# Performance work log

Measured on AMD Instinct MI355X. Metric: run time of the kernel, lower is better.

Reference implementation:

```python
import jax, jax.numpy as jnp
import numpy as np

DM = 512; NH = 8; EL = 3; FACTOR = 3; EPS = 1e-5

def layernorm(x, g, b):
    m = x.mean(-1, keepdims=True)
    v = x.var(-1, keepdims=True)
    return (x - m) / jnp.sqrt(v + EPS) * g + b

def pos_embed(L, d):
    pos = jnp.arange(L, dtype=jnp.float32)[:, None]
    div = jnp.exp(jnp.arange(0, d, 2, dtype=jnp.float32) * (-np.log(10000.0) / d))
    pe = jnp.zeros((L, d), jnp.float32)
    pe = pe.at[:, 0::2].set(jnp.sin(pos * div))
    pe = pe.at[:, 1::2].set(jnp.cos(pos * div))
    return pe

def circ_conv1d(x, w, b=None):
    # x: [B,L,Cin], w: [Cout,Cin,3]; torch Conv1d padding=1, padding_mode='circular'
    xp = jnp.concatenate([x[:, -1:], x, x[:, :1]], axis=1)
    y = jax.lax.conv_general_dilated(xp, w, (1,), 'VALID', dimension_numbers=('NWC', 'OIW', 'NWC'))
    return y if b is None else y + b

def prob_attention(q, k, v, rng):
    # q,k,v: [B,H,L,D] -- Informer ProbSparse attention (non-masked encoder case)
    B, H, L, D = q.shape
    LK = k.shape[2]
    U = min(int(FACTOR * np.ceil(np.log(LK))), LK)   # sampled keys per query
    u = min(int(FACTOR * np.ceil(np.log(L))), L)     # top queries kept
    idx = jax.random.randint(rng, (L, U), 0, LK)     # shared across B,H as in torch
    k_samp = k[:, :, idx]                            # [B,H,L,U,D]
    qk = jnp.einsum('bhld,bhlud->bhlu', q, k_samp)
    M = qk.max(-1) - qk.sum(-1) / LK                 # sparsity measure
    top = jax.lax.top_k(M, u)[1]                     # [B,H,u]
    q_red = jnp.take_along_axis(q, top[..., None], axis=2)
    scores = jnp.einsum('bhud,bhkd->bhuk', q_red, k) / jnp.sqrt(jnp.asarray(D, q.dtype))
    attn = jax.nn.softmax(scores, axis=-1)
    upd = jnp.einsum('bhuk,bhkd->bhud', attn, v)
    ctx = jnp.broadcast_to(v.mean(axis=2, keepdims=True), (B, H, L, D))
    bi = jnp.arange(B)[:, None, None]
    hi = jnp.arange(H)[None, :, None]
    return ctx.at[bi, hi, top].set(upd)

def encoder_layer(x, p, rng):
    Wq_, bq_, Wk_, bk_, Wv_, bv_, Wo_, bo_, w1, b1, w2, b2, g1, be1, g2, be2 = p
    B, L, _ = x.shape
    D = DM // NH
    q = (x @ Wq_.T + bq_).reshape(B, L, NH, D).transpose(0, 2, 1, 3)
    k = (x @ Wk_.T + bk_).reshape(B, L, NH, D).transpose(0, 2, 1, 3)
    v = (x @ Wv_.T + bv_).reshape(B, L, NH, D).transpose(0, 2, 1, 3)
    ctx = prob_attention(q, k, v, rng).transpose(0, 2, 1, 3).reshape(B, L, DM)
    x = x + (ctx @ Wo_.T + bo_)
    x = layernorm(x, g1, be1)
    y = jax.nn.gelu(x @ w1.T + b1, approximate=False)  # pointwise conv1 (k=1)
    y = y @ w2.T + b2                                   # pointwise conv2 (k=1)
    return layernorm(x + y, g2, be2)

def distil_layer(x, w, b, g, beta):
    y = circ_conv1d(x, w, b)                 # Conv1d k=3 circular
    mu = y.mean((0, 1))
    var = y.var((0, 1))                      # BatchNorm1d, training stats
    y = (y - mu) / jnp.sqrt(var + EPS) * g + beta
    y = jax.nn.elu(y)
    # MaxPool1d(kernel=3, stride=2, padding=1)
    return jax.lax.reduce_window(y, -jnp.inf, jax.lax.max, (1, 3, 1), (1, 2, 1), ((0, 0), (1, 1), (0, 0)))

def setup_inputs():
    key = jax.random.key(0)
    ks = jax.random.split(key, 12)
    B, S, CIN, COUT, DFF = 8, 2048, 7, 7, 2048
    r = lambda k, s: jax.random.normal(k, s, jnp.float32)
    return {
        'x_enc': r(ks[0], (B, S, CIN)),
        'tok_w': r(ks[1], (DM, CIN, 3)) * (2.0 / (CIN * 3)) ** 0.5,
        'Wq': r(ks[2], (EL, DM, DM)) * DM ** -0.5, 'bq': jnp.zeros((EL, DM)),
        'Wk': r(ks[3], (EL, DM, DM)) * DM ** -0.5, 'bk': jnp.zeros((EL, DM)),
        'Wv': r(ks[4], (EL, DM, DM)) * DM ** -0.5, 'bv': jnp.zeros((EL, DM)),
        'Wo': r(ks[5], (EL, DM, DM)) * DM ** -0.5, 'bo': jnp.zeros((EL, DM)),
        'conv1_w': r(ks[6], (EL, DFF, DM)) * DM ** -0.5, 'conv1_b': jnp.zeros((EL, DFF)),
        'conv2_w': r(ks[7], (EL, DM, DFF)) * DFF ** -0.5, 'conv2_b': jnp.zeros((EL, DM)),
        'ln1_g': jnp.ones((EL, DM)), 'ln1_b': jnp.zeros((EL, DM)),
        'ln2_g': jnp.ones((EL, DM)), 'ln2_b': jnp.zeros((EL, DM)),
        'dconv_w': r(ks[8], (EL - 1, DM, DM, 3)) * (DM * 3) ** -0.5, 'dconv_b': jnp.zeros((EL - 1, DM)),
        'bn_g': jnp.ones((EL - 1, DM)), 'bn_b': jnp.zeros((EL - 1, DM)),
        'lnf_g': jnp.ones((DM,)), 'lnf_b': jnp.zeros((DM,)),
        'end_w': r(ks[9], (COUT, DM)) * DM ** -0.5, 'end_b': jnp.zeros((COUT,)),
    }

def reference(x_enc, tok_w, Wq, bq, Wk, bk, Wv, bv, Wo, bo, conv1_w, conv1_b, conv2_w, conv2_b, ln1_g, ln1_b, ln2_g, ln2_b, dconv_w, dconv_b, bn_g, bn_b, lnf_g, lnf_b, end_w, end_b):
    x = circ_conv1d(x_enc, tok_w) + pos_embed(x_enc.shape[1], DM)  # DataEmbedding
    base = jax.random.key(42)
    for l in range(EL):
        p = (Wq[l], bq[l], Wk[l], bk[l], Wv[l], bv[l], Wo[l], bo[l],
             conv1_w[l], conv1_b[l], conv2_w[l], conv2_b[l],
             ln1_g[l], ln1_b[l], ln2_g[l], ln2_b[l])
        x = encoder_layer(x, p, jax.random.fold_in(base, l))
        if l < EL - 1:
            x = distil_layer(x, dconv_w[l], dconv_b[l], bn_g[l], bn_b[l])
    x = layernorm(x, lnf_g, lnf_b)
    return x @ end_w.T + end_b  # end_conv2 (Conv1d k=1)
```

## Files before the change

kernel.cpp:

```cpp
#include <hip/hip_runtime.h>
#include <cstdint>
#include <cstddef>

#define DMODEL 512
#define NHEAD 8
#define HD 64

typedef float f32x4 __attribute__((ext_vector_type(4)));
typedef _Float16 f16x8 __attribute__((ext_vector_type(8)));
typedef _Float16 f16x4 __attribute__((ext_vector_type(4)));

__device__ __forceinline__ uint32_t rotl32(uint32_t x, int r) {
  return (x << r) | (x >> (32 - r));
}

__device__ __forceinline__ void tf_block(uint32_t k0, uint32_t k1,
                                         uint32_t& x0, uint32_t& x1) {
  uint32_t ks0 = k0, ks1 = k1, ks2 = k0 ^ k1 ^ 0x1BD11BDAu;
  x0 += ks0; x1 += ks1;
  x0 += x1; x1 = rotl32(x1, 13); x1 ^= x0;
  x0 += x1; x1 = rotl32(x1, 15); x1 ^= x0;
  x0 += x1; x1 = rotl32(x1, 26); x1 ^= x0;
  x0 += x1; x1 = rotl32(x1, 6);  x1 ^= x0;
  x0 += ks1; x1 += ks2 + 1u;
  x0 += x1; x1 = rotl32(x1, 17); x1 ^= x0;
  x0 += x1; x1 = rotl32(x1, 29); x1 ^= x0;
  x0 += x1; x1 = rotl32(x1, 16); x1 ^= x0;
  x0 += x1; x1 = rotl32(x1, 24); x1 ^= x0;
  x0 += ks2; x1 += ks0 + 2u;
  x0 += x1; x1 = rotl32(x1, 13); x1 ^= x0;
  x0 += x1; x1 = rotl32(x1, 15); x1 ^= x0;
  x0 += x1; x1 = rotl32(x1, 26); x1 ^= x0;
  x0 += x1; x1 = rotl32(x1, 6);  x1 ^= x0;
  x0 += ks0; x1 += ks1 + 3u;
  x0 += x1; x1 = rotl32(x1, 17); x1 ^= x0;
  x0 += x1; x1 = rotl32(x1, 29); x1 ^= x0;
  x0 += x1; x1 = rotl32(x1, 16); x1 ^= x0;
  x0 += x1; x1 = rotl32(x1, 24); x1 ^= x0;
  x0 += ks1; x1 += ks2 + 4u;
  x0 += x1; x1 = rotl32(x1, 13); x1 ^= x0;
  x0 += x1; x1 = rotl32(x1, 15); x1 ^= x0;
  x0 += x1; x1 = rotl32(x1, 26); x1 ^= x0;
  x0 += x1; x1 = rotl32(x1, 6);  x1 ^= x0;
  x0 += ks2; x1 += ks0 + 5u;
}

__global__ void idx_kernel(int* __restrict__ idxb, int n, int layer, int mask) {
  int e = blockIdx.x * 256 + threadIdx.x;
  if (e >= n) return;
  uint32_t f0 = 0u, f1 = (uint32_t)layer;
  tf_block(0u, 42u, f0, f1);
  uint32_t s0 = 0u, s1 = 1u;
  tf_block(f0, f1, s0, s1);
  uint32_t x0 = 0u, x1 = (uint32_t)e;
  tf_block(s0, s1, x0, x1);
  uint32_t bits = x0 ^ x1;
  idxb[e] = (int)(bits & (uint32_t)mask);
}

__device__ __forceinline__ float gelu_f(float v) {
  return 0.5f * v * (1.0f + erff(v * 0.7071067811865476f));
}

template <int ACT, int HASR, int CONV, int PART>
__global__ __launch_bounds__(256, 2) void gemm128(
    const float* __restrict__ A, const void* __restrict__ Wsp,
    const float* __restrict__ bias, const float* Rres, float* C,
    int N, int K, int Lmask, int ntx, int nty, int kloop, int ks) {
  __shared__ __align__(16) _Float16 sm[4][128][32];
  const _Float16* Wh = (const _Float16*)Wsp;
  const _Float16* Wl = Wh + (size_t)N * K;
  const int tid = threadIdx.x;
  int blk = blockIdx.x;
  const int tiles = ntx * nty;
  int kb = 0;
  if (PART) { kb = blk / tiles; blk -= kb * tiles; }
  const int koff = kb * kloop;
  const int xcd = blk & 7;
  const int j = blk >> 3;
  const int jr = j / ntx;
  const int row_t = xcd * (nty >> 3) + jr;
  const int col_t = j - jr * ntx;
  const int row0 = row_t * 128, col0 = col_t * 128;

  const int r4 = tid >> 2;
  const int ss = tid & 3;

  const float* Ap0 = A + (size_t)(row0 + r4) * K + koff + ss * 8;
  const float* Ap1 = A + (size_t)(row0 + 64 + r4) * K + koff + ss * 8;
  const _Float16* Wh0 = Wh + (size_t)(col0 + r4) * K + koff + ss * 8;
  const _Float16* Wh1 = Wh + (size_t)(col0 + 64 + r4) * K + koff + ss * 8;
  const _Float16* Wl0 = Wl + (size_t)(col0 + r4) * K + koff + ss * 8;
  const _Float16* Wl1 = Wl + (size_t)(col0 + 64 + r4) * K + koff + ss * 8;
  int tcv0 = 0, bb0 = 0, tcv1 = 0, bb1 = 0;
  if (CONV) {
    int a0 = row0 + r4, a1 = row0 + 64 + r4;
    tcv0 = a0 & Lmask; bb0 = a0 & ~Lmask;
    tcv1 = a1 & Lmask; bb1 = a1 & ~Lmask;
  }

  const int lane = tid & 63;
  const int wv = tid >> 6;
  const int wr = (wv >> 1) << 6;
  const int wc = (wv & 1) << 6;
  const int fr = lane & 15;
  const int fs = lane >> 4;

  f32x4 acc[4][4];
  {
    f32x4 z = {0.f, 0.f, 0.f, 0.f};
#pragma unroll
    for (int r = 0; r < 4; ++r)
#pragma unroll
      for (int c = 0; c < 4; ++c) acc[r][c] = z;
  }

  f32x4 ra[4], rwh[2], rwl[2];

  auto gload = [&](int k0) {
    const float *a0p, *a1p;
    if (CONV) {
      int kabs = koff + k0 + ss * 8;
      int w = kabs >> 9, cq = kabs & 511;
      a0p = A + (size_t)(bb0 | ((tcv0 - 1 + w) & Lmask)) * 512 + cq;
      a1p = A + (size_t)(bb1 | ((tcv1 - 1 + w) & Lmask)) * 512 + cq;
    } else {
      a0p = Ap0 + k0;
      a1p = Ap1 + k0;
    }
    ra[0] = *(const f32x4*)(a0p);
    ra[1] = *(const f32x4*)(a0p + 4);
    ra[2] = *(const f32x4*)(a1p);
    ra[3] = *(const f32x4*)(a1p + 4);
    rwh[0] = *(const f32x4*)(Wh0 + k0);
    rwh[1] = *(const f32x4*)(Wh1 + k0);
    rwl[0] = *(const f32x4*)(Wl0 + k0);
    rwl[1] = *(const f32x4*)(Wl1 + k0);
  };

  const int T = kloop >> 5;
  gload(0);

  for (int it = 0; it < T; ++it) {
#pragma unroll
    for (int p = 0; p < 2; ++p) {
      const int row = (p << 6) + r4;
      const int sl = (ss ^ ((row >> 1) & 3)) << 3;
      float tmp[8];
      *(f32x4*)(tmp) = ra[2 * p];
      *(f32x4*)(tmp + 4) = ra[2 * p + 1];
      _Float16 hv[8], lv[8];
#pragma unroll
      for (int q = 0; q < 8; ++q) {
        _Float16 h = (_Float16)tmp[q];
        hv[q] = h;
        lv[q] = (_Float16)(tmp[q] - (float)h);
      }
      *(f16x8*)&sm[0][row][sl] = *(f16x8*)hv;
      *(f16x8*)&sm[1][row][sl] = *(f16x8*)lv;
      *(f32x4*)&sm[2][row][sl] = rwh[p];
      *(f32x4*)&sm[3][row][sl] = rwl[p];
    }
    __syncthreads();
    if (it + 1 < T) gload((it + 1) << 5);
    f16x8 wfh[4], wfl[4], afh[4], afl[4];
#pragma unroll
    for (int c = 0; c < 4; ++c) {
      const int row = wc + (c << 4) + fr;
      const int sl = (fs ^ ((row >> 1) & 3)) << 3;
      wfh[c] = *(const f16x8*)&sm[2][row][sl];
      wfl[c] = *(const f16x8*)&sm[3][row][sl];
    }
#pragma unroll
    for (int r = 0; r < 4; ++r) {
      const int row = wr + (r << 4) + fr;
      const int sl = (fs ^ ((row >> 1) & 3)) << 3;
      afh[r] = *(const f16x8*)&sm[0][row][sl];
      afl[r] = *(const f16x8*)&sm[1][row][sl];
    }
#pragma unroll
    for (int r = 0; r < 4; ++r)
#pragma unroll
      for (int c = 0; c < 4; ++c) {
        acc[r][c] = __builtin_amdgcn_mfma_f32_16x16x32_f16(afh[r], wfh[c],
                                                           acc[r][c], 0, 0, 0);
        acc[r][c] = __builtin_amdgcn_mfma_f32_16x16x32_f16(afh[r], wfl[c],
                                                           acc[r][c], 0, 0, 0);
        acc[r][c] = __builtin_amdgcn_mfma_f32_16x16x32_f16(afl[r], wfh[c],
                                                           acc[r][c], 0, 0, 0);
      }
    __syncthreads();
  }

  const int crow = fs << 2;
  if (PART) {
    float* Cp = C + (size_t)kb * ((size_t)(nty << 7)) * N;
#pragma unroll
    for (int r = 0; r < 4; ++r) {
      const int m0 = row0 + wr + (r << 4) + crow;
#pragma unroll
      for (int c = 0; c < 4; ++c) {
        const int n0 = col0 + wc + (c << 4) + fr;
#pragma unroll
        for (int q = 0; q < 4; ++q)
          Cp[(size_t)(m0 + q) * N + n0] = acc[r][c][q];
      }
    }
  } else {
#pragma unroll
    for (int r = 0; r < 4; ++r) {
      const int m0 = row0 + wr + (r << 4) + crow;
#pragma unroll
      for (int c = 0; c < 4; ++c) {
        const int n0 = col0 + wc + (c << 4) + fr;
        const float bcol = bias[n0];
#pragma unroll
        for (int q = 0; q < 4; ++q) {
          float v = acc[r][c][q] + bcol;
          if (HASR) v += Rres[(size_t)(m0 + q) * N + n0];
          if (ACT == 1) v = gelu_f(v);
          C[(size_t)(m0 + q) * N + n0] = v;
        }
      }
    }
  }
}

template <int HASR>
__global__ __launch_bounds__(256) void combine_kernel(
    const float* __restrict__ part, const float* __restrict__ bias,
    const float* Rres, float* __restrict__ Cout, size_t MN, int ks) {
  size_t gid = (size_t)blockIdx.x * 256 + threadIdx.x;
  int c = (int)(gid & 511);
  float v = 0.f;
  for (int kb = 0; kb < ks; kb++) v += part[kb * MN + gid];
  v += bias[c];
  if (HASR) v += Rres[gid];
  Cout[gid] = v;
}

__global__ __launch_bounds__(256) void splitw_kernel(const float* __restrict__ w,
                                                     _Float16* __restrict__ o,
                                                     int n) {
  int g = (blockIdx.x * 256 + threadIdx.x) << 2;
  if (g >= n) return;
  f32x4 f = *(const f32x4*)(w + g);
  f16x4 hv, lv;
#pragma unroll
  for (int q = 0; q < 4; ++q) {
    _Float16 h = (_Float16)f[q];
    hv[q] = h;
    lv[q] = (_Float16)(f[q] - (float)h);
  }
  *(f16x4*)(o + g) = hv;
  *(f16x4*)(o + n + g) = lv;
}

__global__ void tokpe_kernel(const float* __restrict__ xe,
                             const float* __restrict__ w,
                             float* __restrict__ out, int S) {
  int gid = blockIdx.x * 256 + threadIdx.x;
  int o = gid & 511;
  int bt = gid >> 9;
  int t = bt % S, b = bt / S;
  float acc = 0.f;
#pragma unroll
  for (int ww = 0; ww < 3; ww++) {
    int tt = t - 1 + ww;
    tt = (tt < 0) ? tt + S : (tt >= S ? tt - S : tt);
    const float* xr = xe + ((size_t)(b * S + tt)) * 7;
#pragma unroll
    for (int i = 0; i < 7; i++) acc += xr[i] * w[o * 21 + i * 3 + ww];
  }
  int i2 = o >> 1;
  float dv = expf((float)(2 * i2) * (-9.210340371976184f / 512.0f));
  float ang = (float)t * dv;
  acc += (o & 1) ? cosf(ang) : sinf(ang);
  out[gid] = acc;
}

__global__ void packw_kernel(const float* __restrict__ dw,
                             _Float16* __restrict__ wp) {
  int gid = blockIdx.x * 256 + threadIdx.x;
  int o = gid / 1536;
  int kk = gid - o * 1536;
  int ww = kk / 512;
  int c = kk - ww * 512;
  float v = dw[((size_t)o * 512 + c) * 3 + ww];
  _Float16 h = (_Float16)v;
  wp[gid] = h;
  wp[786432 + gid] = (_Float16)(v - (float)h);
}

__global__ __launch_bounds__(256, 8) void mscore_kernel(
    const float* __restrict__ Q, const float* __restrict__ Kb,
    const int* __restrict__ idxb, float* __restrict__ Mout, int L, int U) {
  int i = blockIdx.x;
  int b = i & 7;
  int j = i >> 3;
  int tid = threadIdx.x;
  int qd = tid >> 2;
  int q = tid & 3;
  int h = qd & 7;
  int t = j * 8 + (qd >> 3);
  const float* qp = Q + ((size_t)(b * L + t)) * DMODEL + h * HD + q * 4;
  float4 qv0 = *(const float4*)(qp);
  float4 qv1 = *(const float4*)(qp + 16);
  float4 qv2 = *(const float4*)(qp + 32);
  float4 qv3 = *(const float4*)(qp + 48);
  const float* Kh = Kb + (size_t)b * L * DMODEL + h * HD + q * 4;
  const int* ip = idxb + t * U;
  float mx = -3.4e38f, sm = 0.f;
  int kr = ip[0];
  for (int jj = 0; jj < U; jj++) {
    const float* kp = Kh + (size_t)kr * DMODEL;
    float4 k0 = *(const float4*)(kp);
    float4 k1 = *(const float4*)(kp + 16);
    float4 k2 = *(const float4*)(kp + 32);
    float4 k3 = *(const float4*)(kp + 48);
    if (jj + 1 < U) kr = ip[jj + 1];
    float d = qv0.x * k0.x + qv0.y * k0.y + qv0.z * k0.z + qv0.w * k0.w +
              qv1.x * k1.x + qv1.y * k1.y + qv1.z * k1.z + qv1.w * k1.w +
              qv2.x * k2.x + qv2.y * k2.y + qv2.z * k2.z + qv2.w * k2.w +
              qv3.x * k3.x + qv3.y * k3.y + qv3.z * k3.z + qv3.w * k3.w;
    d += __shfl_xor(d, 1);
    d += __shfl_xor(d, 2);
    mx = fmaxf(mx, d);
    sm += d;
  }
  if (q == 0) Mout[(size_t)(b * 8 + h) * L + t] = mx - sm / (float)L;
}

__global__ __launch_bounds__(256) void topk_kernel(const float* __restrict__ Mv,
                                                   int* __restrict__ topb, int L,
                                                   int u) {
  __shared__ float wv_s[4];
  __shared__ int wi_s[4];
  __shared__ int best_s;
// ... 332 lines not shown
    if (t < 0 || t >= L) continue;
    float yv = (z[((size_t)(b * L + t)) * DMODEL + c] - m) * inv * gg + bb;
    yv = (yv > 0.f) ? yv : expm1f(yv);
    best = fmaxf(best, yv);
  }
  out[gid] = best;
}

__global__ __launch_bounds__(64) void end_kernel(const float* __restrict__ xn,
                                                 const float* __restrict__ ew,
                                                 const float* __restrict__ eb,
                                                 float* __restrict__ out) {
  __shared__ float xs[512];
  __shared__ float red[64];
  int row = blockIdx.x, tid = threadIdx.x;
#pragma unroll
  for (int i = 0; i < 8; i++) xs[tid + 64 * i] = xn[(size_t)row * DMODEL + tid + 64 * i];
  __syncthreads();
  for (int c = 0; c < 7; c++) {
    float p = 0.f;
    for (int d = tid; d < 512; d += 64) p += xs[d] * ew[c * DMODEL + d];
    red[tid] = p;
    __syncthreads();
    for (int s = 32; s > 0; s >>= 1) {
      if (tid < s) red[tid] += red[tid + s];
      __syncthreads();
    }
    if (tid == 0) out[row * 7 + c] = red[0] + eb[c];
    __syncthreads();
  }
}

extern "C" void kernel_launch(void* const* d_in, const int* in_sizes, int n_in,
                              void* d_out, int out_size, void* d_ws,
                              size_t ws_size, hipStream_t stream) {
  (void)in_sizes; (void)n_in; (void)out_size;
  const float* x_enc = (const float*)d_in[0];
  const float* tok_w = (const float*)d_in[1];
  const float* Wq = (const float*)d_in[2];
  const float* bq = (const float*)d_in[3];
  const float* Wk = (const float*)d_in[4];
  const float* bk = (const float*)d_in[5];
  const float* Wv = (const float*)d_in[6];
  const float* bv = (const float*)d_in[7];
  const float* Wo = (const float*)d_in[8];
  const float* bo = (const float*)d_in[9];
  const float* w1 = (const float*)d_in[10];
  const float* b1 = (const float*)d_in[11];
  const float* w2 = (const float*)d_in[12];
  const float* b2 = (const float*)d_in[13];
  const float* g1 = (const float*)d_in[14];
  const float* be1 = (const float*)d_in[15];
  const float* g2 = (const float*)d_in[16];
  const float* be2 = (const float*)d_in[17];
  const float* dw = (const float*)d_in[18];
  const float* db = (const float*)d_in[19];
  const float* bng = (const float*)d_in[20];
  const float* bnb = (const float*)d_in[21];
  const float* lnfg = (const float*)d_in[22];
  const float* lnfb = (const float*)d_in[23];
  const float* endw = (const float*)d_in[24];
  const float* endb = (const float*)d_in[25];
  float* out = (float*)d_out;
  char* ws = (char*)d_ws;

  const int NCHMAX = 32;

  size_t o = 0;
  float* buf0 = (float*)(ws + o); o += (size_t)16384 * 512 * 4;
  float* qbuf = (float*)(ws + o); o += (size_t)16384 * 512 * 4;
  float* kbuf = (float*)(ws + o); o += (size_t)16384 * 512 * 4;
  float* wpack = (float*)(ws + o); o += (size_t)512 * 1536 * 4;
  float* Mb    = (float*)(ws + o); o += (size_t)64 * 2048 * 4;
  int*   idxb  = (int*)(ws + o);   o += (size_t)2048 * 24 * 4;
  int*   topb  = (int*)(ws + o);   o += 8192;
  float* qsel  = (float*)(ws + o); o += (size_t)64 * 24 * 64 * 4;
  float* mvg   = (float*)(ws + o); o += (size_t)8 * 512 * 4;
  float* mvWog = (float*)(ws + o); o += (size_t)8 * 512 * 4;
  float* psumx = (float*)(ws + o); o += (size_t)64 * 512 * 4;
  float* psum  = (float*)(ws + o); o += (size_t)128 * 512 * 4;
  float* psq   = (float*)(ws + o); o += (size_t)128 * 512 * 4;
  float* muv   = (float*)(ws + o); o += 2048;
  float* varv  = (float*)(ws + o); o += 2048;
  float* pmb   = (float*)(ws + o); o += (size_t)64 * NCHMAX * 24 * 4;
  float* plb   = (float*)(ws + o); o += (size_t)64 * NCHMAX * 24 * 4;
  float* pOb   = (float*)(ws + o); o += (size_t)64 * NCHMAX * 24 * 64 * 4;
  _Float16* wqs = (_Float16*)(ws + o); o += (size_t)512 * 512 * 4;
  _Float16* w1s = (_Float16*)(ws + o); o += (size_t)2048 * 512 * 4;
  _Float16* w2s = (_Float16*)(ws + o); o += (size_t)512 * 2048 * 4;
  float* partb = (float*)(ws + o); o += (size_t)4 * 4096 * 2048;
  const bool uks = (ws_size >= o);

  const int B = 8;
  const int S = 2048;
  tokpe_kernel<<<B * S * DMODEL / 256, 256, 0, stream>>>(x_enc, tok_w, buf0, S);

  int L = S;
  const int Uarr[3] = {24, 21, 21};
  for (int l = 0; l < 3; l++) {
    int U = Uarr[l];
    int u = Uarr[l];
    int BL = B * L;
    int nty = BL / 128;
    size_t MN = (size_t)BL * 512;
    int gq = 4 * nty;
    int ksq = (gq >= 512 || !uks) ? 1 : (512 / gq);
    int nch = L >> 6;
    idx_kernel<<<(L * U + 255) / 256, 256, 0, stream>>>(idxb, L * U, l, L - 1);

    splitw_kernel<<<256, 256, 0, stream>>>(Wq + (size_t)l * 262144, wqs, 262144);
    if (ksq == 1) {
      gemm128<0, 0, 0, 0><<<gq, 256, 0, stream>>>(
          buf0, wqs, bq + l * 512, nullptr, qbuf, 512, 512, 0, 4, nty, 512, 1);
    } else {
      gemm128<0, 0, 0, 1><<<gq * ksq, 256, 0, stream>>>(
          buf0, wqs, nullptr, nullptr, partb, 512, 512, 0, 4, nty, 512 / ksq,
          ksq);
      combine_kernel<0><<<(unsigned)(MN / 256), 256, 0, stream>>>(
          partb, bq + l * 512, nullptr, qbuf, MN, ksq);
    }
    splitw_kernel<<<256, 256, 0, stream>>>(Wk + (size_t)l * 262144, wqs, 262144);
    if (ksq == 1) {
      gemm128<0, 0, 0, 0><<<gq, 256, 0, stream>>>(
          buf0, wqs, bk + l * 512, nullptr, kbuf, 512, 512, 0, 4, nty, 512, 1);
    } else {
      gemm128<0, 0, 0, 1><<<gq * ksq, 256, 0, stream>>>(
          buf0, wqs, nullptr, nullptr, partb, 512, 512, 0, 4, nty, 512 / ksq,
          ksq);
      combine_kernel<0><<<(unsigned)(MN / 256), 256, 0, stream>>>(
          partb, bk + l * 512, nullptr, kbuf, MN, ksq);
    }
    mscore_kernel<<<L, 256, 0, stream>>>(qbuf, kbuf, idxb, Mb, L, U);
    topk_kernel<<<64, 256, 0, stream>>>(Mb, topb, L, u);
    gatherq_kernel<<<64 * u, 64, 0, stream>>>(qbuf, topb, qsel, L, u);
    xmean_kernel<<<64, 256, 0, stream>>>(buf0, psumx, L);
    mvmake_kernel<<<8, 256, 0, stream>>>(psumx, Wv + (size_t)l * 262144,
                                         bv + l * 512, Wo + (size_t)l * 262144,
                                         bo + l * 512, mvg, mvWog, L);
    splitw_kernel<<<256, 256, 0, stream>>>(Wv + (size_t)l * 262144, wqs, 262144);
    if (ksq == 1) {
      gemm128<0, 0, 0, 0><<<gq, 256, 0, stream>>>(
          buf0, wqs, bv + l * 512, nullptr, qbuf, 512, 512, 0, 4, nty, 512, 1);
    } else {
      gemm128<0, 0, 0, 1><<<gq * ksq, 256, 0, stream>>>(
          buf0, wqs, nullptr, nullptr, partb, 512, 512, 0, 4, nty, 512 / ksq,
          ksq);
      combine_kernel<0><<<(unsigned)(MN / 256), 256, 0, stream>>>(
          partb, bv + l * 512, nullptr, qbuf, MN, ksq);
    }
    attnflash_kernel<<<64 * nch, 256, 0, stream>>>(qsel, kbuf, qbuf, pmb, plb,
                                                   pOb, L, u, nch);
    x1bcast_kernel<<<(unsigned)(MN / 256), 256, 0, stream>>>(buf0, mvWog, kbuf, L);
    deltaWo_kernel<<<64 * u, 256, 0, stream>>>(pmb, plb, pOb, mvg, topb,
                                               Wo + (size_t)l * 262144, kbuf, L,
                                               u, nch);
    ln_kernel<<<BL / 4, 256, 0, stream>>>(kbuf, g1 + l * 512, be1 + l * 512, qbuf);
    splitw_kernel<<<1024, 256, 0, stream>>>(w1 + (size_t)l * 1048576, w1s,
                                            1048576);
    splitw_kernel<<<1024, 256, 0, stream>>>(w2 + (size_t)l * 1048576, w2s,
                                            1048576);
    for (int r0 = 0; r0 < BL; r0 += 4096) {
      gemm128<1, 0, 0, 0><<<16 * 32, 256, 0, stream>>>(
          qbuf + (size_t)r0 * 512, w1s, b1 + l * 2048, nullptr, buf0, 2048, 512,
          0, 16, 32, 512, 1);
      if (uks) {
        gemm128<0, 0, 0, 1><<<4 * 32 * 4, 256, 0, stream>>>(
            buf0, w2s, nullptr, nullptr, partb, 512, 2048, 0, 4, 32, 512, 4);
        combine_kernel<1><<<4096 * 512 / 256, 256, 0, stream>>>(
            partb, b2 + l * 512, qbuf + (size_t)r0 * 512,
            kbuf + (size_t)r0 * 512, (size_t)4096 * 512, 4);
      } else {
        gemm128<0, 1, 0, 0><<<4 * 32, 256, 0, stream>>>(
            buf0, w2s, b2 + l * 512, qbuf + (size_t)r0 * 512,
            kbuf + (size_t)r0 * 512, 512, 2048, 0, 4, 32, 2048, 1);
      }
    }
    ln_kernel<<<BL / 4, 256, 0, stream>>>(kbuf, g2 + l * 512, be2 + l * 512, buf0);

    if (l < 2) {
      packw_kernel<<<512 * 1536 / 256, 256, 0, stream>>>(
          dw + (size_t)l * 512 * 512 * 3, (_Float16*)wpack);
      int ksc = (gq >= 512 || !uks) ? 1 : 2;
      if (ksc == 1) {
        gemm128<0, 0, 1, 0><<<gq, 256, 0, stream>>>(
            buf0, wpack, db + l * 512, nullptr, kbuf, 512, 1536, L - 1, 4, nty,
            1536, 1);
      } else {
        gemm128<0, 0, 1, 1><<<gq * 2, 256, 0, stream>>>(
            buf0, wpack, nullptr, nullptr, partb, 512, 1536, L - 1, 4, nty, 768,
            2);
        combine_kernel<0><<<(unsigned)(MN / 256), 256, 0, stream>>>(
            partb, db + l * 512, nullptr, kbuf, MN, 2);
      }
      int nb = BL / 128;
      bnpart_kernel<<<nb, 256, 0, stream>>>(kbuf, psum, psq, 128);
      bnfin_kernel<<<2, 256, 0, stream>>>(psum, psq, muv, varv, nb, BL);
      bnpool_kernel<<<(BL / 2) * 512 / 256, 256, 0, stream>>>(
          kbuf, muv, varv, bng + l * 512, bnb + l * 512, buf0, L);
      L >>= 1;
    }
  }
  int BL = B * L;
  ln_kernel<<<BL / 4, 256, 0, stream>>>(buf0, lnfg, lnfb, qbuf);
  end_kernel<<<BL, 64, 0, stream>>>(qbuf, endw, endb, out);
}
```

Measured before the change: 1.970 ms.

## Double-buffer LDS tiles in gemm128 to overlap staging with MFMA

Splits the GEMM shared memory into two buffers so the next K-slice is converted and written to LDS while MFMAs run on fragments already loaded into registers. This drops one of the two barriers per iteration and prefetches global data two steps ahead. The cost is doubled LDS (64KB per block) and more live registers, which may reduce occupancy under launch_bounds(256,2).

```diff
diff --git a/kernel.cpp b/kernel.cpp
--- a/kernel.cpp
+++ b/kernel.cpp
@@ -67,7 +67,7 @@
     const float* __restrict__ A, const void* __restrict__ Wsp,
     const float* __restrict__ bias, const float* Rres, float* C,
     int N, int K, int Lmask, int ntx, int nty, int kloop, int ks) {
-  __shared__ __align__(16) _Float16 sm[4][128][32];
+  __shared__ __align__(16) _Float16 sm[2][4][128][32];
   const _Float16* Wh = (const _Float16*)Wsp;
   const _Float16* Wl = Wh + (size_t)N * K;
   const int tid = threadIdx.x;
@@ -116,6 +116,7 @@
   }
 
   f32x4 ra[4], rwh[2], rwl[2];
+  f16x8 wfh[4], wfl[4], afh[4], afl[4];
 
   auto gload = [&](int k0) {
     const float *a0p, *a1p;
@@ -138,10 +139,7 @@
     rwl[1] = *(const f32x4*)(Wl1 + k0);
   };
 
-  const int T = kloop >> 5;
-  gload(0);
-
-  for (int it = 0; it < T; ++it) {
+  auto stage = [&](int buf) {
 #pragma unroll
     for (int p = 0; p < 2; ++p) {
       const int row = (p << 6) + r4;
@@ -156,28 +154,40 @@
         hv[q] = h;
         lv[q] = (_Float16)(tmp[q] - (float)h);
       }
-      *(f16x8*)&sm[0][row][sl] = *(f16x8*)hv;
-      *(f16x8*)&sm[1][row][sl] = *(f16x8*)lv;
-      *(f32x4*)&sm[2][row][sl] = rwh[p];
-      *(f32x4*)&sm[3][row][sl] = rwl[p];
-    }
-    __syncthreads();
-    if (it + 1 < T) gload((it + 1) << 5);
-    f16x8 wfh[4], wfl[4], afh[4], afl[4];
+      *(f16x8*)&sm[buf][0][row][sl] = *(f16x8*)hv;
+      *(f16x8*)&sm[buf][1][row][sl] = *(f16x8*)lv;
+      *(f32x4*)&sm[buf][2][row][sl] = rwh[p];
+      *(f32x4*)&sm[buf][3][row][sl] = rwl[p];
+    }
+  };
+
+  auto readfrags = [&](int buf) {
 #pragma unroll
     for (int c = 0; c < 4; ++c) {
       const int row = wc + (c << 4) + fr;
       const int sl = (fs ^ ((row >> 1) & 3)) << 3;
-      wfh[c] = *(const f16x8*)&sm[2][row][sl];
-      wfl[c] = *(const f16x8*)&sm[3][row][sl];
+      wfh[c] = *(const f16x8*)&sm[buf][2][row][sl];
+      wfl[c] = *(const f16x8*)&sm[buf][3][row][sl];
     }
 #pragma unroll
     for (int r = 0; r < 4; ++r) {
       const int row = wr + (r << 4) + fr;
       const int sl = (fs ^ ((row >> 1) & 3)) << 3;
-      afh[r] = *(const f16x8*)&sm[0][row][sl];
-      afl[r] = *(const f16x8*)&sm[1][row][sl];
-    }
+      afh[r] = *(const f16x8*)&sm[buf][0][row][sl];
+      afl[r] = *(const f16x8*)&sm[buf][1][row][sl];
+    }
+  };
+
+  const int T = kloop >> 5;
+  int cur = 0;
+  gload(0);
+  stage(0);
+  if (T > 1) gload(1 << 5);
+  __syncthreads();
+  readfrags(0);
+
+  for (int it = 0; it < T; ++it) {
+    if (it + 1 < T) stage(cur ^ 1);
 #pragma unroll
     for (int r = 0; r < 4; ++r)
 #pragma unroll
@@ -189,7 +199,12 @@
         acc[r][c] = __builtin_amdgcn_mfma_f32_16x16x32_f16(afl[r], wfh[c],
                                                            acc[r][c], 0, 0, 0);
       }
-    __syncthreads();
+    if (it + 1 < T) {
+      __syncthreads();
+      cur ^= 1;
+      readfrags(cur);
+      if (it + 2 < T) gload((it + 2) << 5);
+    }
   }
 
   const int crow = fs << 2;
```

Result: no change. 1.980 ms, median of 2 (+0.5%).

## Shrink GEMM tile to 64x128 with four waves splitting columns, raise occupancy

Applied to the files above, without the earlier changes.

The split-fp16 GEMM's M tile is halved from 128 to 64 rows. Each of the four waves now covers all 64 rows and a 32-column slice, which cuts accumulators and LDS use so launch bounds can ask for 4 blocks per CU. MFMA calls are grouped by pass and wrapped in s_setprio, and all launch grids and split-K thresholds are doubled to match the new tiling. The goal is more parallelism and occupancy on small-M GEMMs, at the cost of less A/W reuse per tile and more W traffic.

```diff
diff --git a/kernel.cpp b/kernel.cpp
--- a/kernel.cpp
+++ b/kernel.cpp
@@ -63,11 +63,12 @@
 }
 
 template <int ACT, int HASR, int CONV, int PART>
-__global__ __launch_bounds__(256, 2) void gemm128(
+__global__ __launch_bounds__(256, 4) void gemm128(
     const float* __restrict__ A, const void* __restrict__ Wsp,
     const float* __restrict__ bias, const float* Rres, float* C,
     int N, int K, int Lmask, int ntx, int nty, int kloop, int ks) {
-  __shared__ __align__(16) _Float16 sm[4][128][32];
+  __shared__ __align__(16) _Float16 smA[2][64][32];
+  __shared__ __align__(16) _Float16 smW[2][128][32];
   const _Float16* Wh = (const _Float16*)Wsp;
   const _Float16* Wl = Wh + (size_t)N * K;
   const int tid = threadIdx.x;
@@ -81,74 +82,63 @@
   const int jr = j / ntx;
   const int row_t = xcd * (nty >> 3) + jr;
   const int col_t = j - jr * ntx;
-  const int row0 = row_t * 128, col0 = col_t * 128;
+  const int row0 = row_t * 64, col0 = col_t * 128;
 
   const int r4 = tid >> 2;
   const int ss = tid & 3;
 
-  const float* Ap0 = A + (size_t)(row0 + r4) * K + koff + ss * 8;
-  const float* Ap1 = A + (size_t)(row0 + 64 + r4) * K + koff + ss * 8;
+  const float* Ap = A + (size_t)(row0 + r4) * K + koff + ss * 8;
   const _Float16* Wh0 = Wh + (size_t)(col0 + r4) * K + koff + ss * 8;
   const _Float16* Wh1 = Wh + (size_t)(col0 + 64 + r4) * K + koff + ss * 8;
   const _Float16* Wl0 = Wl + (size_t)(col0 + r4) * K + koff + ss * 8;
   const _Float16* Wl1 = Wl + (size_t)(col0 + 64 + r4) * K + koff + ss * 8;
-  int tcv0 = 0, bb0 = 0, tcv1 = 0, bb1 = 0;
+  int tcv = 0, bb = 0;
   if (CONV) {
-    int a0 = row0 + r4, a1 = row0 + 64 + r4;
-    tcv0 = a0 & Lmask; bb0 = a0 & ~Lmask;
-    tcv1 = a1 & Lmask; bb1 = a1 & ~Lmask;
+    int a0 = row0 + r4;
+    tcv = a0 & Lmask; bb = a0 & ~Lmask;
   }
 
   const int lane = tid & 63;
   const int wv = tid >> 6;
-  const int wr = (wv >> 1) << 6;
-  const int wc = (wv & 1) << 6;
+  const int wc = wv << 5;
   const int fr = lane & 15;
   const int fs = lane >> 4;
 
-  f32x4 acc[4][4];
+  f32x4 acc[4][2];
   {
     f32x4 z = {0.f, 0.f, 0.f, 0.f};
 #pragma unroll
     for (int r = 0; r < 4; ++r)
 #pragma unroll
-      for (int c = 0; c < 4; ++c) acc[r][c] = z;
-  }
-
-  f32x4 ra[4], rwh[2], rwl[2];
+      for (int c = 0; c < 2; ++c) acc[r][c] = z;
+  }
+
+  f32x4 ra[2], rwh[2], rwl[2];
+  f16x8 wfh[2], wfl[2], afh[4], afl[4];
 
   auto gload = [&](int k0) {
-    const float *a0p, *a1p;
+    const float* ap;
     if (CONV) {
       int kabs = koff + k0 + ss * 8;
       int w = kabs >> 9, cq = kabs & 511;
-      a0p = A + (size_t)(bb0 | ((tcv0 - 1 + w) & Lmask)) * 512 + cq;
-      a1p = A + (size_t)(bb1 | ((tcv1 - 1 + w) & Lmask)) * 512 + cq;
+      ap = A + (size_t)(bb | ((tcv - 1 + w) & Lmask)) * 512 + cq;
     } else {
-      a0p = Ap0 + k0;
-      a1p = Ap1 + k0;
-    }
-    ra[0] = *(const f32x4*)(a0p);
-    ra[1] = *(const f32x4*)(a0p + 4);
-    ra[2] = *(const f32x4*)(a1p);
-    ra[3] = *(const f32x4*)(a1p + 4);
+      ap = Ap + k0;
+    }
+    ra[0] = *(const f32x4*)(ap);
+    ra[1] = *(const f32x4*)(ap + 4);
     rwh[0] = *(const f32x4*)(Wh0 + k0);
     rwh[1] = *(const f32x4*)(Wh1 + k0);
     rwl[0] = *(const f32x4*)(Wl0 + k0);
     rwl[1] = *(const f32x4*)(Wl1 + k0);
   };
 
-  const int T = kloop >> 5;
-  gload(0);
-
-  for (int it = 0; it < T; ++it) {
-#pragma unroll
-    for (int p = 0; p < 2; ++p) {
-      const int row = (p << 6) + r4;
-      const int sl = (ss ^ ((row >> 1) & 3)) << 3;
+  auto stage = [&]() {
+    {
+      const int sl = (ss ^ ((r4 >> 1) & 3)) << 3;
       float tmp[8];
-      *(f32x4*)(tmp) = ra[2 * p];
-      *(f32x4*)(tmp + 4) = ra[2 * p + 1];
+      *(f32x4*)(tmp) = ra[0];
+      *(f32x4*)(tmp + 4) = ra[1];
       _Float16 hv[8], lv[8];
 #pragma unroll
       for (int q = 0; q < 8; ++q) {
@@ -156,50 +146,74 @@
         hv[q] = h;
         lv[q] = (_Float16)(tmp[q] - (float)h);
       }
-      *(f16x8*)&sm[0][row][sl] = *(f16x8*)hv;
-      *(f16x8*)&sm[1][row][sl] = *(f16x8*)lv;
-      *(f32x4*)&sm[2][row][sl] = rwh[p];
-      *(f32x4*)&sm[3][row][sl] = rwl[p];
-    }
+      *(f16x8*)&smA[0][r4][sl] = *(f16x8*)hv;
+      *(f16x8*)&smA[1][r4][sl] = *(f16x8*)lv;
+    }
+#pragma unroll
+    for (int p = 0; p < 2; ++p) {
+      const int row = (p << 6) + r4;
+      const int sl = (ss ^ ((row >> 1) & 3)) << 3;
+      *(f32x4*)&smW[0][row][sl] = rwh[p];
+      *(f32x4*)&smW[1][row][sl] = rwl[p];
+    }
+  };
+
+  auto readfrags = [&]() {
+#pragma unroll
+    for (int c = 0; c < 2; ++c) {
+      const int row = wc + (c << 4) + fr;
+      const int sl = (fs ^ ((row >> 1) & 3)) << 3;
+      wfh[c] = *(const f16x8*)&smW[0][row][sl];
+      wfl[c] = *(const f16x8*)&smW[1][row][sl];
+    }
+#pragma unroll
+    for (int r = 0; r < 4; ++r) {
+      const int row = (r << 4) + fr;
+      const int sl = (fs ^ ((row >> 1) & 3)) << 3;
+      afh[r] = *(const f16x8*)&smA[0][row][sl];
+      afl[r] = *(const f16x8*)&smA[1][row][sl];
+    }
+  };
+
+  const int T = kloop >> 5;
+  gload(0);
+
+  for (int it = 0; it < T; ++it) {
+    stage();
     __syncthreads();
     if (it + 1 < T) gload((it + 1) << 5);
-    f16x8 wfh[4], wfl[4], afh[4], afl[4];
-#pragma unroll
-    for (int c = 0; c < 4; ++c) {
-      const int row = wc + (c << 4) + fr;
-      const int sl = (fs ^ ((row >> 1) & 3)) << 3;
-      wfh[c] = *(const f16x8*)&sm[2][row][sl];
-      wfl[c] = *(const f16x8*)&sm[3][row][sl];
-    }
-#pragma unroll
-    for (int r = 0; r < 4; ++r) {
-      const int row = wr + (r << 4) + fr;
-      const int sl = (fs ^ ((row >> 1) & 3)) << 3;
-      afh[r] = *(const f16x8*)&sm[0][row][sl];
-      afl[r] = *(const f16x8*)&sm[1][row][sl];
-    }
+    readfrags();
+    __builtin_amdgcn_s_setprio(1);
 #pragma unroll
     for (int r = 0; r < 4; ++r)
 #pragma unroll
-      for (int c = 0; c < 4; ++c) {
+      for (int c = 0; c < 2; ++c)
         acc[r][c] = __builtin_amdgcn_mfma_f32_16x16x32_f16(afh[r], wfh[c],
                                                            acc[r][c], 0, 0, 0);
+#pragma unroll
+    for (int r = 0; r < 4; ++r)
+#pragma unroll
+      for (int c = 0; c < 2; ++c)
         acc[r][c] = __builtin_amdgcn_mfma_f32_16x16x32_f16(afh[r], wfl[c],
                                                            acc[r][c], 0, 0, 0);
+#pragma unroll
+    for (int r = 0; r < 4; ++r)
+#pragma unroll
+      for (int c = 0; c < 2; ++c)
         acc[r][c] = __builtin_amdgcn_mfma_f32_16x16x32_f16(afl[r], wfh[c],
                                                            acc[r][c], 0, 0, 0);
-      }
+    __builtin_amdgcn_s_setprio(0);
     __syncthreads();
   }
 
   const int crow = fs << 2;
   if (PART) {
-    float* Cp = C + (size_t)kb * ((size_t)(nty << 7)) * N;
+    float* Cp = C + (size_t)kb * ((size_t)(nty << 6)) * N;
 #pragma unroll
     for (int r = 0; r < 4; ++r) {
-      const int m0 = row0 + wr + (r << 4) + crow;
-#pragma unroll
-      for (int c = 0; c < 4; ++c) {
+      const int m0 = row0 + (r << 4) + crow;
+#pragma unroll
+      for (int c = 0; c < 2; ++c) {
         const int n0 = col0 + wc + (c << 4) + fr;
 #pragma unroll
         for (int q = 0; q < 4; ++q)
@@ -209,9 +223,9 @@
   } else {
 #pragma unroll
     for (int r = 0; r < 4; ++r) {
-      const int m0 = row0 + wr + (r << 4) + crow;
-#pragma unroll
-      for (int c = 0; c < 4; ++c) {
+      const int m0 = row0 + (r << 4) + crow;
+#pragma unroll
+      for (int c = 0; c < 2; ++c) {
         const int n0 = col0 + wc + (c << 4) + fr;
         const float bcol = bias[n0];
 #pragma unroll
@@ -771,20 +785,20 @@
     int U = Uarr[l];
     int u = Uarr[l];
     int BL = B * L;
-    int nty = BL / 128;
+    int ntyQ = BL >> 6;
     size_t MN = (size_t)BL * 512;
-    int gq = 4 * nty;
-    int ksq = (gq >= 512 || !uks) ? 1 : (512 / gq);
+    int gq = 4 * ntyQ;
+    int ksq = (gq >= 1024 || !uks) ? 1 : (1024 / gq);
     int nch = L >> 6;
     idx_kernel<<<(L * U + 255) / 256, 256, 0, stream>>>(idxb, L * U, l, L - 1);
 
     splitw_kernel<<<256, 256, 0, stream>>>(Wq + (size_t)l * 262144, wqs, 262144);
     if (ksq == 1) {
       gemm128<0, 0, 0, 0><<<gq, 256, 0, stream>>>(
-          buf0, wqs, bq + l * 512, nullptr, qbuf, 512, 512, 0, 4, nty, 512, 1);
+          buf0, wqs, bq + l * 512, nullptr, qbuf, 512, 512, 0, 4, ntyQ, 512, 1);
     } else {
       gemm128<0, 0, 0, 1><<<gq * ksq, 256, 0, stream>>>(
-          buf0, wqs, nullptr, nullptr, partb, 512, 512, 0, 4, nty, 512 / ksq,
+          buf0, wqs, nullptr, nullptr, partb, 512, 512, 0, 4, ntyQ, 512 / ksq,
           ksq);
       combine_kernel<0><<<(unsigned)(MN / 256), 256, 0, stream>>>(
           partb, bq + l * 512, nullptr, qbuf, MN, ksq);
@@ -792,10 +806,10 @@
     splitw_kernel<<<256, 256, 0, stream>>>(Wk + (size_t)l * 262144, wqs, 262144);
     if (ksq == 1) {
       gemm128<0, 0, 0, 0><<<gq, 256, 0, stream>>>(
-          buf0, wqs, bk + l * 512, nullptr, kbuf, 512, 512, 0, 4, nty, 512, 1);
+          buf0, wqs, bk + l * 512, nullptr, kbuf, 512, 512, 0, 4, ntyQ, 512, 1);
     } else {
       gemm128<0, 0, 0, 1><<<gq * ksq, 256, 0, stream>>>(
-          buf0, wqs, nullptr, nullptr, partb, 512, 512, 0, 4, nty, 512 / ksq,
+          buf0, wqs, nullptr, nullptr, partb, 512, 512, 0, 4, ntyQ, 512 / ksq,
           ksq);
       combine_kernel<0><<<(unsigned)(MN / 256), 256, 0, stream>>>(
           partb, bk + l * 512, nullptr, kbuf, MN, ksq);
@@ -810,10 +824,10 @@
     splitw_kernel<<<256, 256, 0, stream>>>(Wv + (size_t)l * 262144, wqs, 262144);
     if (ksq == 1) {
       gemm128<0, 0, 0, 0><<<gq, 256, 0, stream>>>(
-          buf0, wqs, bv + l * 512, nullptr, qbuf, 512, 512, 0, 4, nty, 512, 1);
+          buf0, wqs, bv + l * 512, nullptr, qbuf, 512, 512, 0, 4, ntyQ, 512, 1);
     } else {
       gemm128<0, 0, 0, 1><<<gq * ksq, 256, 0, stream>>>(
-          buf0, wqs, nullptr, nullptr, partb, 512, 512, 0, 4, nty, 512 / ksq,
+          buf0, wqs, nullptr, nullptr, partb, 512, 512, 0, 4, ntyQ, 512 / ksq,
           ksq);
       combine_kernel<0><<<(unsigned)(MN / 256), 256, 0, stream>>>(
           partb, bv + l * 512, nullptr, qbuf, MN, ksq);
@@ -830,19 +844,19 @@
     splitw_kernel<<<1024, 256, 0, stream>>>(w2 + (size_t)l * 1048576, w2s,
                                             1048576);
     for (int r0 = 0; r0 < BL; r0 += 4096) {
-      gemm128<1, 0, 0, 0><<<16 * 32, 256, 0, stream>>>(
+      gemm128<1, 0, 0, 0><<<16 * 64, 256, 0, stream>>>(
           qbuf + (size_t)r0 * 512, w1s, b1 + l * 2048, nullptr, buf0, 2048, 512,
-          0, 16, 32, 512, 1);
+          0, 16, 64, 512, 1);
       if (uks) {
-        gemm128<0, 0, 0, 1><<<4 * 32 * 4, 256, 0, stream>>>(
-            buf0, w2s, nullptr, nullptr, partb, 512, 2048, 0, 4, 32, 512, 4);
+        gemm128<0, 0, 0, 1><<<4 * 64 * 4, 256, 0, stream>>>(
+            buf0, w2s, nullptr, nullptr, partb, 512, 2048, 0, 4, 64, 512, 4);
         combine_kernel<1><<<4096 * 512 / 256, 256, 0, stream>>>(
             partb, b2 + l * 512, qbuf + (size_t)r0 * 512,
             kbuf + (size_t)r0 * 512, (size_t)4096 * 512, 4);
       } else {
-        gemm128<0, 1, 0, 0><<<4 * 32, 256, 0, stream>>>(
+        gemm128<0, 1, 0, 0><<<4 * 64, 256, 0, stream>>>(
             buf0, w2s, b2 + l * 512, qbuf + (size_t)r0 * 512,
-            kbuf + (size_t)r0 * 512, 512, 2048, 0, 4, 32, 2048, 1);
+            kbuf + (size_t)r0 * 512, 512, 2048, 0, 4, 64, 2048, 1);
       }
     }
     ln_kernel<<<BL / 4, 256, 0, stream>>>(kbuf, g2 + l * 512, be2 + l * 512, buf0);
@@ -850,15 +864,15 @@
     if (l < 2) {
       packw_kernel<<<512 * 1536 / 256, 256, 0, stream>>>(
           dw + (size_t)l * 512 * 512 * 3, (_Float16*)wpack);
-      int ksc = (gq >= 512 || !uks) ? 1 : 2;
+      int ksc = (gq >= 1024 || !uks) ? 1 : 2;
       if (ksc == 1) {
         gemm128<0, 0, 1, 0><<<gq, 256, 0, stream>>>(
-            buf0, wpack, db + l * 512, nullptr, kbuf, 512, 1536, L - 1, 4, nty,
+            buf0, wpack, db + l * 512, nullptr, kbuf, 512, 1536, L - 1, 4, ntyQ,
             1536, 1);
       } else {
         gemm128<0, 0, 1, 1><<<gq * 2, 256, 0, stream>>>(
-            buf0, wpack, nullptr, nullptr, partb, 512, 1536, L - 1, 4, nty, 768,
-            2);
+            buf0, wpack, nullptr, nullptr, partb, 512, 1536, L - 1, 4, ntyQ,
+            768, 2);
         combine_kernel<0><<<(unsigned)(MN / 256), 256, 0, stream>>>(
             partb, db + l * 512, nullptr, kbuf, MN, 2);
       }
```

Result: slower. 2.028 ms (+3.0%).

## Fuse QKV projections into one GEMM and use single-pass fp16 for FFN/conv

Applied to the files above, without the earlier changes.

Adds a PREC template parameter: the FFN and distil-conv GEMMs now use a single fp16 MFMA instead of the three-term hi/lo split emulating fp32, cutting MFMA work, LDS traffic and weight loads. Q, K and V projections are merged into one N=1536 GEMM with concatenated weights and bias, writing to three separate outputs. This removes per-projection split-K partial buffers and combine kernels. It trades accuracy in the FFN and conv GEMMs for throughput, and reuses the split-K partial buffer to hold V.

```diff
diff --git a/kernel.cpp b/kernel.cpp
--- a/kernel.cpp
+++ b/kernel.cpp
@@ -62,11 +62,11 @@
   return 0.5f * v * (1.0f + erff(v * 0.7071067811865476f));
 }
 
-template <int ACT, int HASR, int CONV, int PART>
+template <int ACT, int HASR, int CONV, int PART, int PREC, int FUSE3>
 __global__ __launch_bounds__(256, 2) void gemm128(
     const float* __restrict__ A, const void* __restrict__ Wsp,
-    const float* __restrict__ bias, const float* Rres, float* C,
-    int N, int K, int Lmask, int ntx, int nty, int kloop, int ks) {
+    const float* __restrict__ bias, const float* Rres, float* C, float* C2,
+    float* C3, int N, int K, int Lmask, int ntx, int nty, int kloop, int ks) {
   __shared__ __align__(16) _Float16 sm[4][128][32];
   const _Float16* Wh = (const _Float16*)Wsp;
   const _Float16* Wl = Wh + (size_t)N * K;
@@ -134,8 +134,10 @@
     ra[3] = *(const f32x4*)(a1p + 4);
     rwh[0] = *(const f32x4*)(Wh0 + k0);
     rwh[1] = *(const f32x4*)(Wh1 + k0);
-    rwl[0] = *(const f32x4*)(Wl0 + k0);
-    rwl[1] = *(const f32x4*)(Wl1 + k0);
+    if (PREC == 3) {
+      rwl[0] = *(const f32x4*)(Wl0 + k0);
+      rwl[1] = *(const f32x4*)(Wl1 + k0);
+    }
   };
 
   const int T = kloop >> 5;
@@ -154,12 +156,12 @@
       for (int q = 0; q < 8; ++q) {
         _Float16 h = (_Float16)tmp[q];
         hv[q] = h;
-        lv[q] = (_Float16)(tmp[q] - (float)h);
+        if (PREC == 3) lv[q] = (_Float16)(tmp[q] - (float)h);
       }
       *(f16x8*)&sm[0][row][sl] = *(f16x8*)hv;
-      *(f16x8*)&sm[1][row][sl] = *(f16x8*)lv;
+      if (PREC == 3) *(f16x8*)&sm[1][row][sl] = *(f16x8*)lv;
       *(f32x4*)&sm[2][row][sl] = rwh[p];
-      *(f32x4*)&sm[3][row][sl] = rwl[p];
+      if (PREC == 3) *(f32x4*)&sm[3][row][sl] = rwl[p];
     }
     __syncthreads();
     if (it + 1 < T) gload((it + 1) << 5);
@@ -169,14 +171,14 @@
       const int row = wc + (c << 4) + fr;
       const int sl = (fs ^ ((row >> 1) & 3)) << 3;
       wfh[c] = *(const f16x8*)&sm[2][row][sl];
-      wfl[c] = *(const f16x8*)&sm[3][row][sl];
+      if (PREC == 3) wfl[c] = *(const f16x8*)&sm[3][row][sl];
     }
 #pragma unroll
     for (int r = 0; r < 4; ++r) {
       const int row = wr + (r << 4) + fr;
       const int sl = (fs ^ ((row >> 1) & 3)) << 3;
       afh[r] = *(const f16x8*)&sm[0][row][sl];
-      afl[r] = *(const f16x8*)&sm[1][row][sl];
+      if (PREC == 3) afl[r] = *(const f16x8*)&sm[1][row][sl];
     }
 #pragma unroll
     for (int r = 0; r < 4; ++r)
@@ -184,10 +186,12 @@
       for (int c = 0; c < 4; ++c) {
         acc[r][c] = __builtin_amdgcn_mfma_f32_16x16x32_f16(afh[r], wfh[c],
                                                            acc[r][c], 0, 0, 0);
-        acc[r][c] = __builtin_amdgcn_mfma_f32_16x16x32_f16(afh[r], wfl[c],
-                                                           acc[r][c], 0, 0, 0);
-        acc[r][c] = __builtin_amdgcn_mfma_f32_16x16x32_f16(afl[r], wfh[c],
-                                                           acc[r][c], 0, 0, 0);
+        if (PREC == 3) {
+          acc[r][c] = __builtin_amdgcn_mfma_f32_16x16x32_f16(
+              afh[r], wfl[c], acc[r][c], 0, 0, 0);
+          acc[r][c] = __builtin_amdgcn_mfma_f32_16x16x32_f16(
+              afl[r], wfh[c], acc[r][c], 0, 0, 0);
+        }
       }
     __syncthreads();
   }
@@ -204,6 +208,22 @@
 #pragma unroll
         for (int q = 0; q < 4; ++q)
           Cp[(size_t)(m0 + q) * N + n0] = acc[r][c][q];
+      }
+    }
+  } else if (FUSE3) {
+    const int grp = col0 >> 9;
+    float* Cb = (grp == 0) ? C : ((grp == 1) ? C2 : C3);
+#pragma unroll
+    for (int r = 0; r < 4; ++r) {
+      const int m0 = row0 + wr + (r << 4) + crow;
+#pragma unroll
+      for (int c = 0; c < 4; ++c) {
+        const int n0 = col0 + wc + (c << 4) + fr;
+        const int cl = n0 & 511;
+        const float bcol = bias[n0];
+#pragma unroll
+        for (int q = 0; q < 4; ++q)
+          Cb[(size_t)(m0 + q) * 512 + cl] = acc[r][c][q] + bcol;
       }
     }
   } else {
@@ -241,7 +261,7 @@
 
 __global__ __launch_bounds__(256) void splitw_kernel(const float* __restrict__ w,
                                                      _Float16* __restrict__ o,
-                                                     int n) {
+                                                     int n, int ps) {
   int g = (blockIdx.x * 256 + threadIdx.x) << 2;
   if (g >= n) return;
   f32x4 f = *(const f32x4*)(w + g);
@@ -253,7 +273,17 @@
     lv[q] = (_Float16)(f[q] - (float)h);
   }
   *(f16x4*)(o + g) = hv;
-  *(f16x4*)(o + n + g) = lv;
+  *(f16x4*)(o + ps + g) = lv;
+}
+
+__global__ void biascat_kernel(const float* __restrict__ a,
+                               const float* __restrict__ b,
+                               const float* __restrict__ c,
+                               float* __restrict__ o) {
+  int g = blockIdx.x * 256 + threadIdx.x;
+  if (g < 512) o[g] = a[g];
+  else if (g < 1024) o[g] = b[g - 512];
+  else if (g < 1536) o[g] = c[g - 1024];
 }
 
 __global__ void tokpe_kernel(const float* __restrict__ xe,
@@ -752,14 +782,15 @@
   float* psq   = (float*)(ws + o); o += (size_t)128 * 512 * 4;
   float* muv   = (float*)(ws + o); o += 2048;
   float* varv  = (float*)(ws + o); o += 2048;
+  float* biasc = (float*)(ws + o); o += 8192;
   float* pmb   = (float*)(ws + o); o += (size_t)64 * NCHMAX * 24 * 4;
   float* plb   = (float*)(ws + o); o += (size_t)64 * NCHMAX * 24 * 4;
   float* pOb   = (float*)(ws + o); o += (size_t)64 * NCHMAX * 24 * 64 * 4;
-  _Float16* wqs = (_Float16*)(ws + o); o += (size_t)512 * 512 * 4;
   _Float16* w1s = (_Float16*)(ws + o); o += (size_t)2048 * 512 * 4;
   _Float16* w2s = (_Float16*)(ws + o); o += (size_t)512 * 2048 * 4;
   float* partb = (float*)(ws + o); o += (size_t)4 * 4096 * 2048;
   const bool uks = (ws_size >= o);
+  float* vbuf = partb;
 
   const int B = 8;
   const int S = 2048;
@@ -771,35 +802,23 @@
     int U = Uarr[l];
     int u = Uarr[l];
     int BL = B * L;
-    int nty = BL / 128;
+    int nty = BL >> 7;
     size_t MN = (size_t)BL * 512;
-    int gq = 4 * nty;
-    int ksq = (gq >= 512 || !uks) ? 1 : (512 / gq);
     int nch = L >> 6;
     idx_kernel<<<(L * U + 255) / 256, 256, 0, stream>>>(idxb, L * U, l, L - 1);
 
-    splitw_kernel<<<256, 256, 0, stream>>>(Wq + (size_t)l * 262144, wqs, 262144);
-    if (ksq == 1) {
-      gemm128<0, 0, 0, 0><<<gq, 256, 0, stream>>>(
-          buf0, wqs, bq + l * 512, nullptr, qbuf, 512, 512, 0, 4, nty, 512, 1);
-    } else {
-      gemm128<0, 0, 0, 1><<<gq * ksq, 256, 0, stream>>>(
-          buf0, wqs, nullptr, nullptr, partb, 512, 512, 0, 4, nty, 512 / ksq,
-          ksq);
-      combine_kernel<0><<<(unsigned)(MN / 256), 256, 0, stream>>>(
-          partb, bq + l * 512, nullptr, qbuf, MN, ksq);
-    }
-    splitw_kernel<<<256, 256, 0, stream>>>(Wk + (size_t)l * 262144, wqs, 262144);
-    if (ksq == 1) {
-      gemm128<0, 0, 0, 0><<<gq, 256, 0, stream>>>(
-          buf0, wqs, bk + l * 512, nullptr, kbuf, 512, 512, 0, 4, nty, 512, 1);
-    } else {
-      gemm128<0, 0, 0, 1><<<gq * ksq, 256, 0, stream>>>(
-          buf0, wqs, nullptr, nullptr, partb, 512, 512, 0, 4, nty, 512 / ksq,
-          ksq);
-      combine_kernel<0><<<(unsigned)(MN / 256), 256, 0, stream>>>(
-          partb, bk + l * 512, nullptr, kbuf, MN, ksq);
-    }
+    splitw_kernel<<<256, 256, 0, stream>>>(Wq + (size_t)l * 262144, w1s,
+                                           262144, 786432);
+    splitw_kernel<<<256, 256, 0, stream>>>(Wk + (size_t)l * 262144,
+                                           w1s + 262144, 262144, 786432);
+    splitw_kernel<<<256, 256, 0, stream>>>(Wv + (size_t)l * 262144,
+                                           w1s + 524288, 262144, 786432);
+    biascat_kernel<<<6, 256, 0, stream>>>(bq + l * 512, bk + l * 512,
+                                          bv + l * 512, biasc);
+    gemm128<0, 0, 0, 0, 3, 1><<<nty * 12, 256, 0, stream>>>(
+        buf0, w1s, biasc, nullptr, qbuf, kbuf, vbuf, 1536, 512, 0, 12, nty,
+        512, 1);
+
     mscore_kernel<<<L, 256, 0, stream>>>(qbuf, kbuf, idxb, Mb, L, U);
     topk_kernel<<<64, 256, 0, stream>>>(Mb, topb, L, u);
     gatherq_kernel<<<64 * u, 64, 0, stream>>>(qbuf, topb, qsel, L, u);
@@ -807,18 +826,7 @@
     mvmake_kernel<<<8, 256, 0, stream>>>(psumx, Wv + (size_t)l * 262144,
                                          bv + l * 512, Wo + (size_t)l * 262144,
                                          bo + l * 512, mvg, mvWog, L);
-    splitw_kernel<<<256, 256, 0, stream>>>(Wv + (size_t)l * 262144, wqs, 262144);
-    if (ksq == 1) {
-      gemm128<0, 0, 0, 0><<<gq, 256, 0, stream>>>(
-          buf0, wqs, bv + l * 512, nullptr, qbuf, 512, 512, 0, 4, nty, 512, 1);
-    } else {
-      gemm128<0, 0, 0, 1><<<gq * ksq, 256, 0, stream>>>(
-          buf0, wqs, nullptr, nullptr, partb, 512, 512, 0, 4, nty, 512 / ksq,
-          ksq);
-      combine_kernel<0><<<(unsigned)(MN / 256), 256, 0, stream>>>(
-          partb, bv + l * 512, nullptr, qbuf, MN, ksq);
-    }
-    attnflash_kernel<<<64 * nch, 256, 0, stream>>>(qsel, kbuf, qbuf, pmb, plb,
+    attnflash_kernel<<<64 * nch, 256, 0, stream>>>(qsel, kbuf, vbuf, pmb, plb,
                                                    pOb, L, u, nch);
     x1bcast_kernel<<<(unsigned)(MN / 256), 256, 0, stream>>>(buf0, mvWog, kbuf, L);
     deltaWo_kernel<<<64 * u, 256, 0, stream>>>(pmb, plb, pOb, mvg, topb,
@@ -826,23 +834,25 @@
                                                u, nch);
     ln_kernel<<<BL / 4, 256, 0, stream>>>(kbuf, g1 + l * 512, be1 + l * 512, qbuf);
     splitw_kernel<<<1024, 256, 0, stream>>>(w1 + (size_t)l * 1048576, w1s,
-                                            1048576);
+                                            1048576, 1048576);
     splitw_kernel<<<1024, 256, 0, stream>>>(w2 + (size_t)l * 1048576, w2s,
-                                            1048576);
+                                            1048576, 1048576);
     for (int r0 = 0; r0 < BL; r0 += 4096) {
-      gemm128<1, 0, 0, 0><<<16 * 32, 256, 0, stream>>>(
-          qbuf + (size_t)r0 * 512, w1s, b1 + l * 2048, nullptr, buf0, 2048, 512,
-          0, 16, 32, 512, 1);
+      gemm128<1, 0, 0, 0, 1, 0><<<16 * 32, 256, 0, stream>>>(
+          qbuf + (size_t)r0 * 512, w1s, b1 + l * 2048, nullptr, buf0, nullptr,
+          nullptr, 2048, 512, 0, 16, 32, 512, 1);
       if (uks) {
-        gemm128<0, 0, 0, 1><<<4 * 32 * 4, 256, 0, stream>>>(
-            buf0, w2s, nullptr, nullptr, partb, 512, 2048, 0, 4, 32, 512, 4);
+        gemm128<0, 0, 0, 1, 1, 0><<<4 * 32 * 4, 256, 0, stream>>>(
+            buf0, w2s, nullptr, nullptr, partb, nullptr, nullptr, 512, 2048, 0,
+            4, 32, 512, 4);
         combine_kernel<1><<<4096 * 512 / 256, 256, 0, stream>>>(
             partb, b2 + l * 512, qbuf + (size_t)r0 * 512,
             kbuf + (size_t)r0 * 512, (size_t)4096 * 512, 4);
       } else {
-        gemm128<0, 1, 0, 0><<<4 * 32, 256, 0, stream>>>(
+        gemm128<0, 1, 0, 0, 1, 0><<<4 * 32, 256, 0, stream>>>(
             buf0, w2s, b2 + l * 512, qbuf + (size_t)r0 * 512,
-            kbuf + (size_t)r0 * 512, 512, 2048, 0, 4, 32, 2048, 1);
+            kbuf + (size_t)r0 * 512, nullptr, nullptr, 512, 2048, 0, 4, 32,
+            2048, 1);
       }
     }
     ln_kernel<<<BL / 4, 256, 0, stream>>>(kbuf, g2 + l * 512, be2 + l * 512, buf0);
@@ -850,15 +860,16 @@
     if (l < 2) {
       packw_kernel<<<512 * 1536 / 256, 256, 0, stream>>>(
           dw + (size_t)l * 512 * 512 * 3, (_Float16*)wpack);
-      int ksc = (gq >= 512 || !uks) ? 1 : 2;
+      int gqc = 4 * nty;
+      int ksc = (gqc >= 512 || !uks) ? 1 : 2;
       if (ksc == 1) {
-        gemm128<0, 0, 1, 0><<<gq, 256, 0, stream>>>(
-            buf0, wpack, db + l * 512, nullptr, kbuf, 512, 1536, L - 1, 4, nty,
-            1536, 1);
+        gemm128<0, 0, 1, 0, 1, 0><<<gqc, 256, 0, stream>>>(
+            buf0, wpack, db + l * 512, nullptr, kbuf, nullptr, nullptr, 512,
+            1536, L - 1, 4, nty, 1536, 1);
       } else {
-        gemm128<0, 0, 1, 1><<<gq * 2, 256, 0, stream>>>(
-            buf0, wpack, nullptr, nullptr, partb, 512, 1536, L - 1, 4, nty, 768,
-            2);
+        gemm128<0, 0, 1, 1, 1, 0><<<gqc * 2, 256, 0, stream>>>(
+            buf0, wpack, nullptr, nullptr, partb, nullptr, nullptr, 512, 1536,
+            L - 1, 4, nty, 768, 2);
         combine_kernel<0><<<(unsigned)(MN / 256), 256, 0, stream>>>(
             partb, db + l * 512, nullptr, kbuf, MN, 2);
       }
```

Result: faster. 1.663 ms, median of 2 (-15.6%).
